# Performance work log

Measured on AMD Instinct MI355X. Metric: run time of the kernel, lower is better.

## Reference

```python
import jax, jax.numpy as jnp
import numpy as np

NUM_FREQ = 32
MAX_POS = 10000.0
COORD_DIM = 3
EMB_DIM = COORD_DIM * NUM_FREQ * 2  # 192
KIN = 2 * EMB_DIM                   # 384
C = 32
T = 4
N_Y = 50000
N_X = 32768
K = 8
E = N_X * K
MLP_DIMS = [KIN, 128, 256, 128, C]


def sinusoidal_embed(p):
    # transformer-style sinusoidal embedding: [n, d] -> [n, d*NUM_FREQ*2]
    freqs = (1.0 / MAX_POS) ** (jnp.arange(NUM_FREQ, dtype=p.dtype) / NUM_FREQ)
    ang = p[..., None] * freqs                       # [n, d, nf]
    emb = jnp.stack([jnp.sin(ang), jnp.cos(ang)], axis=-1)  # [n, d, nf, 2]
    return emb.reshape(p.shape[0], -1)


def setup_inputs() -> dict:
    key = jax.random.key(0)
    ks = jax.random.split(key, 16)
    inp = {
        "y": jax.random.uniform(ks[0], (N_Y, COORD_DIM), dtype=jnp.float32),
        "x": jax.random.uniform(ks[1], (N_X, COORD_DIM), dtype=jnp.float32),
        "f_y": jax.random.normal(ks[2], (T, N_Y, C), dtype=jnp.float32),
        "neighbors_index": jax.random.randint(ks[3], (E,), 0, N_Y, dtype=jnp.int64),
    }
    # channel MLP params: 384 -> 128 -> 256 -> 128 -> 32, gelu between layers
    for i in range(4):
        fan_in, fan_out = MLP_DIMS[i], MLP_DIMS[i + 1]
        s = 1.0 / np.sqrt(fan_in)
        inp[f"W{i}"] = jax.random.uniform(ks[4 + 2 * i], (fan_in, fan_out), jnp.float32, -s, s)
        inp[f"b{i}"] = jax.random.uniform(ks[5 + 2 * i], (fan_out,), jnp.float32, -s, s)
    return inp


def reference(y, x, f_y, neighbors_index, W0, b0, W1, b1, W2, b2, W3, b3):
    n_x = x.shape[0]
    k = neighbors_index.shape[0] // n_x
    y_emb = sinusoidal_embed(y)            # [n_y, 192]
    x_emb = sinusoidal_embed(x)            # [n_x, 192]
    rep = y_emb[neighbors_index]           # [E, 192] gather per edge
    slf = jnp.repeat(x_emb, k, axis=0)     # [E, 192] query embedding per edge
    h = jnp.concatenate([rep, slf], axis=-1)  # [E, 384]
    h = jax.nn.gelu(h @ W0 + b0)
    h = jax.nn.gelu(h @ W1 + b1)
    h = jax.nn.gelu(h @ W2 + b2)
    kern = h @ W3 + b3                     # [E, C] kernel values
    in_feat = f_y[:, neighbors_index, :]   # [T, E, C] gathered source features
    prod = kern[None, :, :] * in_feat      # linear transform: k(x,y) * f(y)
    # reduction='sum' over each query's neighborhood (uniform K segments)
    out = prod.reshape(f_y.shape[0], n_x, k, -1).sum(axis=2)  # [T, n_x, C]
    return out
```

## Files before the change

### kernel.cpp

```cpp
#include <hip/hip_runtime.h>
#include <stdint.h>

#define EMB_DIM 192
#define CDIM 32
#define TDIM 4
#define N_Y 50000
#define N_X 32768
#define KNBR 8
#define ECNT (N_X*KNBR)

#define H1S 134
#define H2S 262
#define KS  33
#define ES  200

#define PREP_TW 272
#define PREP_Y0 PREP_TW
#define PREP_X0 (PREP_TW + 782)
#define PREP_NB (PREP_TW + 782 + 512)

typedef __attribute__((ext_vector_type(8))) short bf16x8;
typedef __attribute__((ext_vector_type(4))) float f32x4;

static __device__ __forceinline__ short f2bf(float f){
  unsigned u = __float_as_uint(f);
  return (short)((u + 0x7FFFu) >> 16);
}
static __device__ __forceinline__ unsigned pk_bf16(float lo, float hi){
  return ((__float_as_uint(lo) + 0x7FFFu) >> 16) |
         ((((__float_as_uint(hi) + 0x7FFFu) >> 16)) << 16);
}
static __device__ __forceinline__ float geluf(float x){
  float x2 = x * x;
  float u  = __builtin_fmaf(0.044715f, x2, 1.0f);
  float p  = x * -1.5957691216057308f;
  float e  = __expf(p * u);
  return x * __builtin_amdgcn_rcpf(1.0f + e);
}

__global__ __launch_bounds__(256, 2) void prep_all(
    const float* __restrict__ ypts, const float* __restrict__ xpts,
    const float* __restrict__ W0, const float* __restrict__ b0,
    const float* __restrict__ W1, const float* __restrict__ W2,
    const float* __restrict__ W3,
    short* __restrict__ w1t, short* __restrict__ w2t, short* __restrict__ w3t,
    short* __restrict__ c_y, float* __restrict__ c_x)
{
  const int tid = threadIdx.x;
  if (blockIdx.x < PREP_TW) {
    int id = blockIdx.x * 256 + tid;
    if (id < 32768) {
      int n = id >> 7, k = id & 127;
      w1t[id] = f2bf(W1[k * 256 + n]);
    } else if (id < 65536) {
      int loc = id - 32768; int n = loc >> 8, k = loc & 255;
      w2t[loc] = f2bf(W2[k * 128 + n]);
    } else if (id < 69632) {
      int loc = id - 65536; int n = loc >> 7, k = loc & 127;
      w3t[loc] = f2bf(W3[k * 32 + n]);
    }
    return;
  }

  __shared__ __attribute__((aligned(16))) short s_e[64 * ES];
  const bool isY = blockIdx.x < PREP_X0;
  const int row0 = isY ? (blockIdx.x - PREP_Y0) * 64 : (blockIdx.x - PREP_X0) * 64;
  const int wave = tid >> 6, lane = tid & 63;
  const int quad = lane >> 4, l15 = lane & 15;
  const float* W0h = W0 + (isY ? 0 : 192 * 128);

  short bv[2][48];
  #pragma unroll
  for (int nt = 0; nt < 2; ++nt) {
    int n = wave * 32 + nt * 16 + l15;
    #pragma unroll
    for (int ch = 0; ch < 6; ++ch)
      #pragma unroll
      for (int j = 0; j < 8; ++j)
        bv[nt][ch * 8 + j] = f2bf(W0h[(size_t)(ch * 32 + quad * 8 + j) * 128 + n]);
  }

  {
    const int r = tid >> 2, q = tid & 3;
    const int grow = row0 + r;
    const bool valid = isY ? (grow < N_Y) : true;
    const float* src = isY ? (ypts + (size_t)grow * 3) : (xpts + (size_t)grow * 3);
    float c[3] = {0.f, 0.f, 0.f};
    if (valid) { c[0] = src[0]; c[1] = src[1]; c[2] = src[2]; }
    #pragma unroll
    for (int j = 0; j < 24; ++j) {
      int p = q * 24 + j;
      int d = p >> 5, i = p & 31;
      float f = __expf(-0.28782313662425575f * (float)i);
      float rev = c[d] * f * 0.15915494309189535f;
      float s  = __builtin_amdgcn_sinf(rev);
      float co = __builtin_amdgcn_cosf(rev);
      *(unsigned*)&s_e[r * ES + d * 64 + 2 * i] = pk_bf16(s, co);
    }
  }
  __syncthreads();

  f32x4 acc[4][2];
  #pragma unroll
  for (int mt = 0; mt < 4; ++mt)
    #pragma unroll
    for (int nt = 0; nt < 2; ++nt) acc[mt][nt] = (f32x4){0.f, 0.f, 0.f, 0.f};
  #pragma unroll
  for (int ch = 0; ch < 6; ++ch) {
    bf16x8 a[4];
    #pragma unroll
    for (int mt = 0; mt < 4; ++mt)
      a[mt] = *(const bf16x8*)&s_e[(mt * 16 + l15) * ES + ch * 32 + quad * 8];
    #pragma unroll
    for (int mt = 0; mt < 4; ++mt)
      #pragma unroll
      for (int nt = 0; nt < 2; ++nt)
        acc[mt][nt] = __builtin_amdgcn_mfma_f32_16x16x32_bf16(
            a[mt], *(const bf16x8*)&bv[nt][ch * 8], acc[mt][nt], 0, 0, 0);
  }
  #pragma unroll
  for (int nt = 0; nt < 2; ++nt) {
    int col = wave * 32 + nt * 16 + l15;
    float bias = isY ? 0.f : b0[col];
    #pragma unroll
    for (int mt = 0; mt < 4; ++mt)
      #pragma unroll
      for (int rg = 0; rg < 4; ++rg) {
        int grow = row0 + mt * 16 + quad * 4 + rg;
        if (isY) { if (grow < N_Y) c_y[(size_t)grow * 128 + col] = f2bf(acc[mt][nt][rg]); }
        else     { c_x[(size_t)grow * 128 + col] = acc[mt][nt][rg] + bias; }
      }
  }
}

__global__ __launch_bounds__(256, 3) void fused_edge(
    const short* __restrict__ c_y, const float* __restrict__ c_x,
    const int* __restrict__ nidx, const float* __restrict__ f_y,
    const short* __restrict__ w1t, const float* __restrict__ b1,
    const short* __restrict__ w2t, const float* __restrict__ b2,
    const short* __restrict__ w3t, const float* __restrict__ b3,
    float* __restrict__ out)
{
  __shared__ __attribute__((aligned(16))) char smem[50688];
  short* s_h2   = (short*)smem;
  float* s_kern = (float*)smem;
  short* s_h1   = (short*)(smem + 33536);

  const int tid  = threadIdx.x;
  const int e0   = blockIdx.x * 64;
  const int wave = tid >> 6, lane = tid & 63;
  const int quad = lane >> 4, l15 = lane & 15;

  {
    const int r = tid >> 2, q = tid & 3;
    const int idx = nidx[e0 + r];
    const uint4*  cyp = (const uint4*)(c_y + (size_t)idx * 128 + q * 32);
    const float4* cxp = (const float4*)(c_x + (size_t)((e0 + r) >> 3) * 128 + q * 32);
    uint4  cyv[4];
    float4 cxv[8];
    #pragma unroll
    for (int i = 0; i < 4; ++i) cyv[i] = cyp[i];
    #pragma unroll
    for (int i = 0; i < 8; ++i) cxv[i] = cxp[i];
    const float* cxa = (const float*)cxv;
    const unsigned* cya = (const unsigned*)cyv;
    unsigned pk[16];
    #pragma unroll
    for (int jj = 0; jj < 16; ++jj) {
      unsigned u = cya[jj];
      float lo = __uint_as_float(u << 16)         + cxa[2 * jj];
      float hi = __uint_as_float(u & 0xffff0000u) + cxa[2 * jj + 1];
      pk[jj] = pk_bf16(geluf(lo), geluf(hi));
    }
    uint4* dst = (uint4*)&s_h1[r * H1S + q * 32];
    #pragma unroll
    for (int jj = 0; jj < 4; ++jj)
      dst[jj] = *(uint4*)&pk[jj * 4];
  }
  __syncthreads();

  {
    f32x4 acc1[4][4];
    #pragma unroll
    for (int mt = 0; mt < 4; ++mt)
      #pragma unroll
      for (int nt = 0; nt < 4; ++nt) acc1[mt][nt] = (f32x4){0.f, 0.f, 0.f, 0.f};
    #pragma unroll
    for (int ch = 0; ch < 4; ++ch) {
      bf16x8 a[4], b[4];
      #pragma unroll
      for (int mt = 0; mt < 4; ++mt)
        a[mt] = *(const bf16x8*)&s_h1[(mt * 16 + l15) * H1S + ch * 32 + quad * 8];
      #pragma unroll
      for (int nt = 0; nt < 4; ++nt)
        b[nt] = *(const bf16x8*)&w1t[(size_t)(wave * 64 + nt * 16 + l15) * 128 + ch * 32 + quad * 8];
      #pragma unroll
      for (int mt = 0; mt < 4; ++mt)
        #pragma unroll
        for (int nt = 0; nt < 4; ++nt)
          acc1[mt][nt] = __builtin_amdgcn_mfma_f32_16x16x32_bf16(a[mt], b[nt], acc1[mt][nt], 0, 0, 0);
    }
    #pragma unroll
    for (int nt = 0; nt < 4; ++nt) {
      int col = wave * 64 + nt * 16 + l15;
      float bias = b1[col];
      #pragma unroll
      for (int mt = 0; mt < 4; ++mt)
        #pragma unroll
        for (int rg = 0; rg < 4; ++rg) {
          int row = mt * 16 + quad * 4 + rg;
          s_h2[row * H2S + col] = f2bf(geluf(acc1[mt][nt][rg] + bias));
        }
    }
  }
  __syncthreads();

  {
    f32x4 acc2[4][2];
    #pragma unroll
    for (int mt = 0; mt < 4; ++mt)
      #pragma unroll
      for (int nt = 0; nt < 2; ++nt) acc2[mt][nt] = (f32x4){0.f, 0.f, 0.f, 0.f};
    #pragma unroll
    for (int ch = 0; ch < 8; ++ch) {
      bf16x8 a[4], b[2];
      #pragma unroll
      for (int mt = 0; mt < 4; ++mt)
        a[mt] = *(const bf16x8*)&s_h2[(mt * 16 + l15) * H2S + ch * 32 + quad * 8];
      #pragma unroll
      for (int nt = 0; nt < 2; ++nt)
        b[nt] = *(const bf16x8*)&w2t[(size_t)(wave * 32 + nt * 16 + l15) * 256 + ch * 32 + quad * 8];
      #pragma unroll
      for (int mt = 0; mt < 4; ++mt)
        #pragma unroll
        for (int nt = 0; nt < 2; ++nt)
          acc2[mt][nt] = __builtin_amdgcn_mfma_f32_16x16x32_bf16(a[mt], b[nt], acc2[mt][nt], 0, 0, 0);
    }
    #pragma unroll
    for (int nt = 0; nt < 2; ++nt) {
      int col = wave * 32 + nt * 16 + l15;
      float bias = b2[col];
      #pragma unroll
      for (int mt = 0; mt < 4; ++mt)
        #pragma unroll
        for (int rg = 0; rg < 4; ++rg) {
          int row = mt * 16 + quad * 4 + rg;
          s_h1[row * H1S + col] = f2bf(geluf(acc2[mt][nt][rg] + bias));
        }
    }
  }
  __syncthreads();

  {
    f32x4 acc3[2];
    acc3[0] = (f32x4){0.f, 0.f, 0.f, 0.f};
    acc3[1] = (f32x4){0.f, 0.f, 0.f, 0.f};
    #pragma unroll
    for (int ch = 0; ch < 4; ++ch) {
      bf16x8 a3 = *(const bf16x8*)&s_h1[(wave * 16 + l15) * H1S + ch * 32 + quad * 8];
      #pragma unroll
      for (int nt = 0; nt < 2; ++nt) {
        bf16x8 b3f = *(const bf16x8*)&w3t[(size_t)(nt * 16 + l15) * 128 + ch * 32 + quad * 8];
        acc3[nt] = __builtin_amdgcn_mfma_f32_16x16x32_bf16(a3, b3f, acc3[nt], 0, 0, 0);
      }
    }
    #pragma unroll
    for (int nt = 0; nt < 2; ++nt) {
      int col = nt * 16 + l15;
      float bias = b3[col];
      #pragma unroll
      for (int rg = 0; rg < 4; ++rg) {
        int row = wave * 16 + quad * 4 + rg;
        s_kern[row * KS + col] = acc3[nt][rg] + bias;
      }
    }
  }
  __syncthreads();

  {
    const int xloc = tid >> 5;
    const int c    = tid & 31;
    float acc[TDIM] = {0.f, 0.f, 0.f, 0.f};
    const int ebase = xloc * 8;
    #pragma unroll
    for (int j = 0; j < KNBR; ++j) {
      float kv = s_kern[(ebase + j) * KS + c];
      int idx = nidx[e0 + ebase + j];
      const float* fp = f_y + (size_t)idx * CDIM + c;
      #pragma unroll
      for (int t = 0; t < TDIM; ++t)
        acc[t] += kv * fp[(size_t)t * N_Y * CDIM];
    }
    const int xg = blockIdx.x * 8 + xloc;
    #pragma unroll
    for (int t = 0; t < TDIM; ++t)
      out[((size_t)t * N_X + xg) * CDIM + c] = acc[t];
  }
}

extern "C" void kernel_launch(void* const* d_in, const int* in_sizes, int n_in,
                              void* d_out, int out_size, void* d_ws, size_t ws_size,
                              hipStream_t stream)
{
  const float* y   = (const float*)d_in[0];
  const float* x   = (const float*)d_in[1];
  const float* f_y = (const float*)d_in[2];
  const int*  nidx = (const int*)d_in[3];
  const float* W0 = (const float*)d_in[4];  const float* b0 = (const float*)d_in[5];
  const float* W1 = (const float*)d_in[6];  const float* b1 = (const float*)d_in[7];
  const float* W2 = (const float*)d_in[8];  const float* b2 = (const float*)d_in[9];
  const float* W3 = (const float*)d_in[10]; const float* b3 = (const float*)d_in[11];

  char* ws = (char*)d_ws;
  short* c_y  = (short*)(ws + 0);
  float* c_x  = (float*)(ws + 12800000);
  short* w1t  = (short*)(ws + 29577216);
  short* w2t  = (short*)(ws + 29642752);
  short* w3t  = (short*)(ws + 29708288);

  hipLaunchKernelGGL(prep_all, dim3(PREP_NB), dim3(256), 0, stream,
                     y, x, W0, b0, W1, W2, W3, w1t, w2t, w3t, c_y, c_x);
  hipLaunchKernelGGL(fused_edge, dim3(ECNT / 64), dim3(256), 0, stream,
                     c_y, c_x, nidx, f_y, w1t, b1, w2t, b2, w3t, b3, (float*)d_out);
}
```

Baseline: 240.9 us.

## Give each wave its own 16-edge patch and drop block-wide barriers in edge MLP

Restructures the fused edge kernel so each wave independently processes 16 edges through all MLP layers, using a private LDS patch instead of block-shared tiles. Layer-1 A fragments are built directly in registers from the gathered c_y/c_x, which skips the LDS staging round trip. Removes all __syncthreads, shrinks LDS from ~50KB to ~34KB, and raises launch bounds to 4 blocks per SM. In exchange, each wave now reads all W1/W2 weight fragments itself, which means more global/L2 weight traffic per edge and more registers per wave.

Result: slower. 366.7 us (+52.2%).

```diff
diff --git a/kernel.cpp b/kernel.cpp
--- a/kernel.cpp
+++ b/kernel.cpp
@@ -9,10 +9,11 @@
 #define KNBR 8
 #define ECNT (N_X*KNBR)
 
-#define H1S 134
-#define H2S 262
-#define KS  33
 #define ES  200
+
+#define PS  264
+#define PBYTES (16*PS*2)
+#define KFS 20
 
 #define PREP_TW 272
 #define PREP_Y0 PREP_TW
@@ -133,7 +134,7 @@
   }
 }
 
-__global__ __launch_bounds__(256, 3) void fused_edge(
+__global__ __launch_bounds__(256, 4) void fused_edge(
     const short* __restrict__ c_y, const float* __restrict__ c_x,
     const int* __restrict__ nidx, const float* __restrict__ f_y,
     const short* __restrict__ w1t, const float* __restrict__ b1,
@@ -141,160 +142,122 @@
     const short* __restrict__ w3t, const float* __restrict__ b3,
     float* __restrict__ out)
 {
-  __shared__ __attribute__((aligned(16))) char smem[50688];
-  short* s_h2   = (short*)smem;
-  float* s_kern = (float*)smem;
-  short* s_h1   = (short*)(smem + 33536);
-
+  __shared__ __attribute__((aligned(16))) char smem[4][PBYTES];
   const int tid  = threadIdx.x;
-  const int e0   = blockIdx.x * 64;
   const int wave = tid >> 6, lane = tid & 63;
   const int quad = lane >> 4, l15 = lane & 15;
-
+  short* patch = (short*)smem[wave];
+
+  const int ew0 = blockIdx.x * 64 + wave * 16;
+
+  bf16x8 af[4];
   {
-    const int r = tid >> 2, q = tid & 3;
-    const int idx = nidx[e0 + r];
-    const uint4*  cyp = (const uint4*)(c_y + (size_t)idx * 128 + q * 32);
-    const float4* cxp = (const float4*)(c_x + (size_t)((e0 + r) >> 3) * 128 + q * 32);
-    uint4  cyv[4];
-    float4 cxv[8];
-    #pragma unroll
-    for (int i = 0; i < 4; ++i) cyv[i] = cyp[i];
-    #pragma unroll
-    for (int i = 0; i < 8; ++i) cxv[i] = cxp[i];
-    const float* cxa = (const float*)cxv;
-    const unsigned* cya = (const unsigned*)cyv;
-    unsigned pk[16];
-    #pragma unroll
-    for (int jj = 0; jj < 16; ++jj) {
-      unsigned u = cya[jj];
-      float lo = __uint_as_float(u << 16)         + cxa[2 * jj];
-      float hi = __uint_as_float(u & 0xffff0000u) + cxa[2 * jj + 1];
-      pk[jj] = pk_bf16(geluf(lo), geluf(hi));
-    }
-    uint4* dst = (uint4*)&s_h1[r * H1S + q * 32];
-    #pragma unroll
-    for (int jj = 0; jj < 4; ++jj)
-      dst[jj] = *(uint4*)&pk[jj * 4];
-  }
-  __syncthreads();
+    const int idx = nidx[ew0 + l15];
+    const short* cyr = c_y + (size_t)idx * 128 + quad * 8;
+    const float* cxr = c_x + (size_t)((ew0 + l15) >> 3) * 128 + quad * 8;
+    #pragma unroll
+    for (int ch = 0; ch < 4; ++ch) {
+      uint4 cy  = *(const uint4*)(cyr + ch * 32);
+      float4 c0 = *(const float4*)(cxr + ch * 32);
+      float4 c1 = *(const float4*)(cxr + ch * 32 + 4);
+      const unsigned* cu = (const unsigned*)&cy;
+      float cf[8] = {c0.x, c0.y, c0.z, c0.w, c1.x, c1.y, c1.z, c1.w};
+      unsigned pk[4];
+      #pragma unroll
+      for (int p = 0; p < 4; ++p) {
+        unsigned u = cu[p];
+        float lo = __uint_as_float(u << 16)         + cf[2 * p];
+        float hi = __uint_as_float(u & 0xffff0000u) + cf[2 * p + 1];
+        pk[p] = pk_bf16(geluf(lo), geluf(hi));
+      }
+      af[ch] = *(bf16x8*)pk;
+    }
+  }
+
+  #pragma unroll
+  for (int h = 0; h < 2; ++h) {
+    f32x4 acc[8];
+    #pragma unroll
+    for (int nt = 0; nt < 8; ++nt) acc[nt] = (f32x4){0.f, 0.f, 0.f, 0.f};
+    #pragma unroll
+    for (int ch = 0; ch < 4; ++ch)
+      #pragma unroll
+      for (int nt = 0; nt < 8; ++nt) {
+        bf16x8 b = *(const bf16x8*)&w1t[(size_t)((h * 8 + nt) * 16 + l15) * 128 + ch * 32 + quad * 8];
+        acc[nt] = __builtin_amdgcn_mfma_f32_16x16x32_bf16(af[ch], b, acc[nt], 0, 0, 0);
+      }
+    #pragma unroll
+    for (int nt = 0; nt < 8; ++nt) {
+      int col = (h * 8 + nt) * 16 + l15;
+      float bias = b1[col];
+      #pragma unroll
+      for (int rg = 0; rg < 4; ++rg)
+        patch[(quad * 4 + rg) * PS + col] = f2bf(geluf(acc[nt][rg] + bias));
+    }
+  }
+
+  f32x4 acc2[8];
+  #pragma unroll
+  for (int nt = 0; nt < 8; ++nt) acc2[nt] = (f32x4){0.f, 0.f, 0.f, 0.f};
+  #pragma unroll
+  for (int ch = 0; ch < 8; ++ch) {
+    bf16x8 a = *(const bf16x8*)&patch[l15 * PS + ch * 32 + quad * 8];
+    #pragma unroll
+    for (int nt = 0; nt < 8; ++nt) {
+      bf16x8 b = *(const bf16x8*)&w2t[(size_t)(nt * 16 + l15) * 256 + ch * 32 + quad * 8];
+      acc2[nt] = __builtin_amdgcn_mfma_f32_16x16x32_bf16(a, b, acc2[nt], 0, 0, 0);
+    }
+  }
+  #pragma unroll
+  for (int nt = 0; nt < 8; ++nt) {
+    int col = nt * 16 + l15;
+    float bias = b2[col];
+    #pragma unroll
+    for (int rg = 0; rg < 4; ++rg)
+      patch[(quad * 4 + rg) * PS + col] = f2bf(geluf(acc2[nt][rg] + bias));
+  }
+
+  f32x4 acc3[2];
+  acc3[0] = (f32x4){0.f, 0.f, 0.f, 0.f};
+  acc3[1] = (f32x4){0.f, 0.f, 0.f, 0.f};
+  #pragma unroll
+  for (int ch = 0; ch < 4; ++ch) {
+    bf16x8 a = *(const bf16x8*)&patch[l15 * PS + ch * 32 + quad * 8];
+    #pragma unroll
+    for (int nt = 0; nt < 2; ++nt) {
+      bf16x8 b = *(const bf16x8*)&w3t[(size_t)(nt * 16 + l15) * 128 + ch * 32 + quad * 8];
+      acc3[nt] = __builtin_amdgcn_mfma_f32_16x16x32_bf16(a, b, acc3[nt], 0, 0, 0);
+    }
+  }
+  float* kf = (float*)patch;
+  #pragma unroll
+  for (int nt = 0; nt < 2; ++nt) {
+    int col = nt * 16 + l15;
+    float bias = b3[col];
+    f32x4 v;
+    #pragma unroll
+    for (int rg = 0; rg < 4; ++rg) v[rg] = acc3[nt][rg] + bias;
+    *(f32x4*)&kf[col * KFS + quad * 4] = v;
+  }
 
   {
-    f32x4 acc1[4][4];
-    #pragma unroll
-    for (int mt = 0; mt < 4; ++mt)
-      #pragma unroll
-      for (int nt = 0; nt < 4; ++nt) acc1[mt][nt] = (f32x4){0.f, 0.f, 0.f, 0.f};
-    #pragma unroll
-    for (int ch = 0; ch < 4; ++ch) {
-      bf16x8 a[4], b[4];
-      #pragma unroll
-      for (int mt = 0; mt < 4; ++mt)
-        a[mt] = *(const bf16x8*)&s_h1[(mt * 16 + l15) * H1S + ch * 32 + quad * 8];
-      #pragma unroll
-      for (int nt = 0; nt < 4; ++nt)
-        b[nt] = *(const bf16x8*)&w1t[(size_t)(wave * 64 + nt * 16 + l15) * 128 + ch * 32 + quad * 8];
-      #pragma unroll
-      for (int mt = 0; mt < 4; ++mt)
-        #pragma unroll
-        for (int nt = 0; nt < 4; ++nt)
-          acc1[mt][nt] = __builtin_amdgcn_mfma_f32_16x16x32_bf16(a[mt], b[nt], acc1[mt][nt], 0, 0, 0);
-    }
-    #pragma unroll
-    for (int nt = 0; nt < 4; ++nt) {
-      int col = wave * 64 + nt * 16 + l15;
-      float bias = b1[col];
-      #pragma unroll
-      for (int mt = 0; mt < 4; ++mt)
-        #pragma unroll
-        for (int rg = 0; rg < 4; ++rg) {
-          int row = mt * 16 + quad * 4 + rg;
-          s_h2[row * H2S + col] = f2bf(geluf(acc1[mt][nt][rg] + bias));
-        }
-    }
-  }
-  __syncthreads();
-
-  {
-    f32x4 acc2[4][2];
-    #pragma unroll
-    for (int mt = 0; mt < 4; ++mt)
-      #pragma unroll
-      for (int nt = 0; nt < 2; ++nt) acc2[mt][nt] = (f32x4){0.f, 0.f, 0.f, 0.f};
-    #pragma unroll
-    for (int ch = 0; ch < 8; ++ch) {
-      bf16x8 a[4], b[2];
-      #pragma unroll
-      for (int mt = 0; mt < 4; ++mt)
-        a[mt] = *(const bf16x8*)&s_h2[(mt * 16 + l15) * H2S + ch * 32 + quad * 8];
-      #pragma unroll
-      for (int nt = 0; nt < 2; ++nt)
-        b[nt] = *(const bf16x8*)&w2t[(size_t)(wave * 32 + nt * 16 + l15) * 256 + ch * 32 + quad * 8];
-      #pragma unroll
-      for (int mt = 0; mt < 4; ++mt)
-        #pragma unroll
-        for (int nt = 0; nt < 2; ++nt)
-          acc2[mt][nt] = __builtin_amdgcn_mfma_f32_16x16x32_bf16(a[mt], b[nt], acc2[mt][nt], 0, 0, 0);
-    }
-    #pragma unroll
-    for (int nt = 0; nt < 2; ++nt) {
-      int col = wave * 32 + nt * 16 + l15;
-      float bias = b2[col];
-      #pragma unroll
-      for (int mt = 0; mt < 4; ++mt)
-        #pragma unroll
-        for (int rg = 0; rg < 4; ++rg) {
-          int row = mt * 16 + quad * 4 + rg;
-          s_h1[row * H1S + col] = f2bf(geluf(acc2[mt][nt][rg] + bias));
-        }
-    }
-  }
-  __syncthreads();
-
-  {
-    f32x4 acc3[2];
-    acc3[0] = (f32x4){0.f, 0.f, 0.f, 0.f};
-    acc3[1] = (f32x4){0.f, 0.f, 0.f, 0.f};
-    #pragma unroll
-    for (int ch = 0; ch < 4; ++ch) {
-      bf16x8 a3 = *(const bf16x8*)&s_h1[(wave * 16 + l15) * H1S + ch * 32 + quad * 8];
-      #pragma unroll
-      for (int nt = 0; nt < 2; ++nt) {
-        bf16x8 b3f = *(const bf16x8*)&w3t[(size_t)(nt * 16 + l15) * 128 + ch * 32 + quad * 8];
-        acc3[nt] = __builtin_amdgcn_mfma_f32_16x16x32_bf16(a3, b3f, acc3[nt], 0, 0, 0);
-      }
-    }
-    #pragma unroll
-    for (int nt = 0; nt < 2; ++nt) {
-      int col = nt * 16 + l15;
-      float bias = b3[col];
-      #pragma unroll
-      for (int rg = 0; rg < 4; ++rg) {
-        int row = wave * 16 + quad * 4 + rg;
-        s_kern[row * KS + col] = acc3[nt][rg] + bias;
-      }
-    }
-  }
-  __syncthreads();
-
-  {
-    const int xloc = tid >> 5;
-    const int c    = tid & 31;
+    const int xl = lane >> 5, cc = lane & 31;
+    f32x4 k0 = *(const f32x4*)&kf[cc * KFS + xl * 8];
+    f32x4 k1 = *(const f32x4*)&kf[cc * KFS + xl * 8 + 4];
     float acc[TDIM] = {0.f, 0.f, 0.f, 0.f};
-    const int ebase = xloc * 8;
     #pragma unroll
     for (int j = 0; j < KNBR; ++j) {
-      float kv = s_kern[(ebase + j) * KS + c];
-      int idx = nidx[e0 + ebase + j];
-      const float* fp = f_y + (size_t)idx * CDIM + c;
+      int idxj = nidx[ew0 + xl * 8 + j];
+      const float* fp = f_y + (size_t)idxj * CDIM + cc;
+      float kv = (j < 4) ? k0[j] : k1[j - 4];
       #pragma unroll
       for (int t = 0; t < TDIM; ++t)
         acc[t] += kv * fp[(size_t)t * N_Y * CDIM];
     }
-    const int xg = blockIdx.x * 8 + xloc;
+    const int xg = blockIdx.x * 8 + wave * 2 + xl;
     #pragma unroll
     for (int t = 0; t < TDIM; ++t)
-      out[((size_t)t * N_X + xg) * CDIM + c] = acc[t];
+      out[((size_t)t * N_X + xg) * CDIM + cc] = acc[t];
   }
 }
 
```
